# Kernel optimization log

Hardware: AMD Instinct MI355X
Metric: run time of the kernel (lower is better)

## Reference

```python
import jax, jax.numpy as jnp
import numpy as np

B, T, E, H, L = 8, 4096, 1024, 16, 64  # batch, seq, embed, heads, local window
HD = E // H


def setup_inputs() -> dict:
    key = jax.random.key(0)
    ks = jax.random.split(key, 5)
    s = 1.0 / np.sqrt(E).astype(np.float32)
    x = jax.random.normal(ks[0], (B, T, E), dtype=jnp.float32)
    W_qkv = jax.random.normal(ks[1], (3 * E, E), dtype=jnp.float32) * s
    b_qkv = jnp.zeros((3 * E,), dtype=jnp.float32)
    W_out = jax.random.normal(ks[2], (E, E), dtype=jnp.float32) * s
    b_out = jnp.zeros((E,), dtype=jnp.float32)
    return {"x": x, "W_qkv": W_qkv, "b_qkv": b_qkv, "W_out": W_out, "b_out": b_out}


def reference(x, W_qkv, b_qkv, W_out, b_out):
    b, t, e = x.shape
    scaling = HD ** (-0.5)
    # T is already a multiple of L, so need_pad = 0 (matches torch path)
    qkv = x @ W_qkv.T + b_qkv                      # (B,T,3E)
    q, k, v = jnp.split(qkv, 3, axis=-1)           # each (B,T,E)
    q = q * scaling

    def to_blocks(a):
        # (B,T,E) -> (B,H,T/L,L,HD); matches torch view/transpose sequence
        return a.reshape(b, t, H, HD).transpose(0, 2, 1, 3).reshape(b, H, t // L, L, HD)

    qb, kb, vb = to_blocks(q), to_blocks(k), to_blocks(v)
    attn = jax.nn.softmax(jnp.einsum('bhnld,bhnmd->bhnlm', qb, kb), axis=-1)
    out = jnp.einsum('bhnlm,bhnmd->bhnld', attn, vb)  # (B,H,N,L,HD)
    out = out.reshape(b, H, t, HD).transpose(0, 2, 1, 3).reshape(b, t, e)
    return out @ W_out.T + b_out
```

## Files before the change

kernel.cpp:

```cpp
#include <hip/hip_runtime.h>
#include <hip/hip_bf16.h>

typedef __hip_bfloat16 bf16;
typedef __attribute__((ext_vector_type(8))) short short8;
typedef __attribute__((ext_vector_type(4))) float f32x4;

__device__ __forceinline__ void gload_lds16(const void* g, void* l) {
    __builtin_amdgcn_global_load_lds(
        (const __attribute__((address_space(1))) void*)g,
        (__attribute__((address_space(3))) void*)l, 16, 0, 0);
}

__device__ __forceinline__ void store_out(bf16* p, float v)  { *p = __float2bfloat16(v); }
__device__ __forceinline__ void store_out(float* p, float v) { *p = v; }

__global__ __launch_bounds__(256)
void cvt_f32_bf16(const float* __restrict__ in, bf16* __restrict__ out, long n)
{
    const long i = ((long)blockIdx.x * 256 + threadIdx.x) * 8;
    if (i + 8 > n) return;
    float4 a = *(const float4*)(in + i);
    float4 b = *(const float4*)(in + i + 4);
    bf16 o[8];
    o[0] = __float2bfloat16(a.x); o[1] = __float2bfloat16(a.y);
    o[2] = __float2bfloat16(a.z); o[3] = __float2bfloat16(a.w);
    o[4] = __float2bfloat16(b.x); o[5] = __float2bfloat16(b.y);
    o[6] = __float2bfloat16(b.z); o[7] = __float2bfloat16(b.w);
    *(uint4*)(out + i) = *(const uint4*)o;
}

template <typename OutT>
__global__ __launch_bounds__(512, 2)
void gemm256(const bf16* __restrict__ A, const bf16* __restrict__ Bt,
             const float* __restrict__ bias, OutT* __restrict__ C,
             int N, int K, int gxt)
{
    __shared__ bf16 As[4][8192];
    __shared__ bf16 Bs[4][8192];

    const int nwg  = gridDim.x;
    const int orig = blockIdx.x;
    const int qq = nwg >> 3, rr = nwg & 7, xc = orig & 7;
    const int wg = (xc < rr ? xc * (qq + 1) : rr * (qq + 1) + (xc - rr) * qq)
                 + (orig >> 3);
    const long m0 = (long)(wg / gxt) * 256;
    const long n0 = (long)(wg % gxt) * 256;

    const int tid = threadIdx.x;
    const int wv  = tid >> 6;
    const int ln  = tid & 63;
    const int l15 = ln & 15;
    const int qd  = ln >> 4;
    const int wm  = wv >> 2, wn = wv & 3;

    const int sl = (qd ^ ((l15 >> 1) & 3)) << 3;

    const int r0  = tid >> 2;
    const int c0s = (((tid & 3) ^ ((tid >> 3) & 3))) << 3;
    const bf16* gA0 = A  + (m0 + r0) * K + c0s;
    const bf16* gA1 = A  + (m0 + 128 + r0) * K + c0s;
    const bf16* gB0 = Bt + (n0 + r0) * K + c0s;
    const bf16* gB1 = Bt + (n0 + 128 + r0) * K + c0s;
    const int lw = wv * 512;

    const int NT = K >> 5;

#define STAGE_A(bb, src) do { \
        gload_lds16(gA0 + (src) * 32, &As[bb][lw]); \
        gload_lds16(gA1 + (src) * 32, &As[bb][4096 + lw]); } while (0)
#define STAGE_B(bb, src) do { \
        gload_lds16(gB0 + (src) * 32, &Bs[bb][lw]); \
        gload_lds16(gB1 + (src) * 32, &Bs[bb][4096 + lw]); } while (0)

    {
        const int s1 = 1 < NT ? 1 : 0;
        const int s2 = 2 < NT ? 2 : 0;
        STAGE_A(0, 0);  STAGE_B(0, 0);
        STAGE_A(1, s1); STAGE_B(1, s1);
        STAGE_A(2, s2); STAGE_B(2, s2);
    }

    f32x4 acc[8][4] = {};

    for (int kt = 0; kt < NT; ++kt) {
        const int b   = kt & 3;
        const int ks  = kt + 3;
        const int bb  = ks & 3;
        const int src = ks < NT ? ks : 0;

        asm volatile("s_waitcnt vmcnt(8)" ::: "memory");
        __builtin_amdgcn_s_barrier();
        asm volatile("" ::: "memory");

        const bf16* Ab = As[b];
        const bf16* Bb = Bs[b];

        short8 af[4], bf[4];
#pragma unroll
        for (int mi = 0; mi < 4; ++mi)
            af[mi] = *(const short8*)&Ab[(wm * 128 + mi * 16 + l15) * 32 + sl];
#pragma unroll
        for (int ni = 0; ni < 4; ++ni)
            bf[ni] = *(const short8*)&Bb[(wn * 64 + ni * 16 + l15) * 32 + sl];
        STAGE_A(bb, src);
        __builtin_amdgcn_s_barrier();
        asm volatile("s_waitcnt lgkmcnt(0)" ::: "memory");
        __builtin_amdgcn_sched_barrier(0);
        __builtin_amdgcn_s_setprio(1);
#pragma unroll
        for (int mi = 0; mi < 4; ++mi)
#pragma unroll
            for (int ni = 0; ni < 4; ++ni)
                acc[mi][ni] = __builtin_amdgcn_mfma_f32_16x16x32_bf16(
                    af[mi], bf[ni], acc[mi][ni], 0, 0, 0);
        __builtin_amdgcn_s_setprio(0);

#pragma unroll
        for (int mi = 0; mi < 4; ++mi)
            af[mi] = *(const short8*)&Ab[(wm * 128 + (mi + 4) * 16 + l15) * 32 + sl];
        STAGE_B(bb, src);
        __builtin_amdgcn_s_barrier();
        asm volatile("s_waitcnt lgkmcnt(0)" ::: "memory");
        __builtin_amdgcn_sched_barrier(0);
        __builtin_amdgcn_s_setprio(1);
#pragma unroll
        for (int mi = 0; mi < 4; ++mi)
#pragma unroll
            for (int ni = 0; ni < 4; ++ni)
                acc[mi + 4][ni] = __builtin_amdgcn_mfma_f32_16x16x32_bf16(
                    af[mi], bf[ni], acc[mi + 4][ni], 0, 0, 0);
        __builtin_amdgcn_s_setprio(0);
    }
#undef STAGE_A
#undef STAGE_B

    const long ccol = n0 + wn * 64;
    float bsv[4];
#pragma unroll
    for (int ni = 0; ni < 4; ++ni)
        bsv[ni] = bias[ccol + ni * 16 + l15];
#pragma unroll
    for (int mi = 0; mi < 8; ++mi) {
#pragma unroll
        for (int r = 0; r < 4; ++r) {
            const long row = m0 + wm * 128 + mi * 16 + qd * 4 + r;
            OutT* cp = C + row * N + ccol + l15;
#pragma unroll
            for (int ni = 0; ni < 4; ++ni)
                store_out(cp + ni * 16, acc[mi][ni][r] + bsv[ni]);
        }
    }
}

#define LROW 72

__global__ __launch_bounds__(256)
void attn_local(const bf16* __restrict__ qkv, bf16* __restrict__ out)
{
    __shared__ bf16 Qs[64 * LROW];
    __shared__ bf16 Ks[64 * LROW];
    __shared__ bf16 Vt[64 * LROW];
    __shared__ bf16 Ps[64 * LROW];

    const int cb = blockIdx.x;
    const int h  = blockIdx.y;
    const int tid = threadIdx.x;

    const long qoff = (long)cb * 64 * 3072 + h * 64;

#pragma unroll
    for (int p = 0; p < 2; ++p) {
        const int e = (p * 256 + tid) * 8;
        const int tk = e >> 6, cl = e & 63;
        const long g = qoff + (long)tk * 3072 + cl;
        *(uint4*)&Qs[tk * LROW + cl] = *(const uint4*)&qkv[g];
        *(uint4*)&Ks[tk * LROW + cl] = *(const uint4*)&qkv[g + 1024];
        uint4 vv = *(const uint4*)&qkv[g + 2048];
        const bf16* vp = (const bf16*)&vv;
#pragma unroll
        for (int j = 0; j < 8; ++j)
            Vt[(cl + j) * LROW + tk] = vp[j];
    }
    __syncthreads();

    const int wv = tid >> 6, ln = tid & 63, l15 = ln & 15, qd = ln >> 4;

    f32x4 sacc[4] = {};
#pragma unroll
    for (int kk = 0; kk < 64; kk += 32) {
        short8 aq = *(const short8*)&Qs[(wv * 16 + l15) * LROW + kk + qd * 8];
#pragma unroll
        for (int ni = 0; ni < 4; ++ni) {
            short8 bk = *(const short8*)&Ks[(ni * 16 + l15) * LROW + kk + qd * 8];
            sacc[ni] = __builtin_amdgcn_mfma_f32_16x16x32_bf16(aq, bk, sacc[ni], 0, 0, 0);
        }
    }

    float linv[4];
#pragma unroll
    for (int r = 0; r < 4; ++r) {
        float m = -3.4e38f;
#pragma unroll
        for (int ni = 0; ni < 4; ++ni) m = fmaxf(m, sacc[ni][r]);
#pragma unroll
        for (int off = 1; off < 16; off <<= 1) m = fmaxf(m, __shfl_xor(m, off));
        float s = 0.f, pv[4];
#pragma unroll
        for (int ni = 0; ni < 4; ++ni) {
            pv[ni] = __expf(0.125f * (sacc[ni][r] - m));
            s += pv[ni];
        }
#pragma unroll
        for (int off = 1; off < 16; off <<= 1) s += __shfl_xor(s, off);
        linv[r] = 1.f / s;
        const int row = wv * 16 + qd * 4 + r;
#pragma unroll
        for (int ni = 0; ni < 4; ++ni)
            Ps[row * LROW + ni * 16 + l15] = __float2bfloat16(pv[ni]);
    }
    __syncthreads();

    f32x4 oacc[4] = {};
#pragma unroll
    for (int kk = 0; kk < 64; kk += 32) {
        short8 ap = *(const short8*)&Ps[(wv * 16 + l15) * LROW + kk + qd * 8];
#pragma unroll
        for (int ni = 0; ni < 4; ++ni) {
            short8 bv = *(const short8*)&Vt[(ni * 16 + l15) * LROW + kk + qd * 8];
            oacc[ni] = __builtin_amdgcn_mfma_f32_16x16x32_bf16(ap, bv, oacc[ni], 0, 0, 0);
        }
    }

    const long obase = (long)cb * 64 * 1024 + h * 64;
#pragma unroll
    for (int r = 0; r < 4; ++r) {
        const int row = wv * 16 + qd * 4 + r;
#pragma unroll
        for (int ni = 0; ni < 4; ++ni)
            out[obase + (long)row * 1024 + ni * 16 + l15] =
                __float2bfloat16(oacc[ni][r] * linv[r]);
    }
}

extern "C" void kernel_launch(void* const* d_in, const int* in_sizes, int n_in,
                              void* d_out, int out_size, void* d_ws, size_t ws_size,
                              hipStream_t stream) {
    const float* x     = (const float*)d_in[0];
    const float* W_qkv = (const float*)d_in[1];
    const float* b_qkv = (const float*)d_in[2];
    const float* W_out = (const float*)d_in[3];
    const float* b_out = (const float*)d_in[4];
    float* out = (float*)d_out;

    bf16* Wqkv_b = (bf16*)d_ws;
    bf16* Wout_b = Wqkv_b + (size_t)3072 * 1024;
    bf16* chunk0 = Wout_b + (size_t)1024 * 1024;
    const size_t fixed_bytes = ((size_t)3072 * 1024 + (size_t)1024 * 1024) * 2;

    static const int cands[8] = {32768, 16384, 8192, 4096, 2048, 1024, 512, 256};
    int CH = 256;
    for (int i = 0; i < 8; ++i)
        if (fixed_bytes + (size_t)cands[i] * 10240 <= ws_size) { CH = cands[i]; break; }

    bf16* xb    = chunk0;
    bf16* qkvb  = xb + (size_t)CH * 1024;
    bf16* attnb = qkvb + (size_t)CH * 3072;

    const dim3 blk(256);
    const dim3 gblk(512);

    cvt_f32_bf16<<<dim3((3072 * 1024) / 2048), blk, 0, stream>>>(W_qkv, Wqkv_b, 3072 * 1024);
    cvt_f32_bf16<<<dim3((1024 * 1024) / 2048), blk, 0, stream>>>(W_out, Wout_b, 1024 * 1024);

    const int mt = CH / 256;

    for (int c0 = 0; c0 < 32768; c0 += CH) {
        const long ne = (long)CH * 1024;
        cvt_f32_bf16<<<dim3((int)(ne / 2048)), blk, 0, stream>>>(x + (size_t)c0 * 1024, xb, ne);
        gemm256<bf16><<<dim3(mt * (3072 / 256)), gblk, 0, stream>>>(
            xb, Wqkv_b, b_qkv, qkvb, 3072, 1024, 3072 / 256);
        attn_local<<<dim3(CH / 64, 16), blk, 0, stream>>>(qkvb, attnb);
        gemm256<float><<<dim3(mt * (1024 / 256)), gblk, 0, stream>>>(
            attnb, Wout_b, b_out, out + (size_t)c0 * 1024, 1024, 1024, 1024 / 256);
    }
}
```

Measured before the change: 586.5 us.

## Software-pipeline LDS fragment loads across k-tiles in the bf16 GEMM loop

The GEMM main loop now loads the next k-tile's A and B fragments from LDS while the current MFMAs run. It ping-pongs two B register sets and unrolls the loop by two. The per-iteration synchronisation drops from three barriers to one, with a looser vmcnt wait. The goal is to hide LDS read latency and barrier stalls behind matrix-core work. In exchange it uses more registers and drops the guards for small K, so it assumes at least three k-tiles and an even tile count.

```diff
diff --git a/kernel.cpp b/kernel.cpp
--- a/kernel.cpp
+++ b/kernel.cpp
@@ -72,65 +72,77 @@
         gload_lds16(gB0 + (src) * 32, &Bs[bb][lw]); \
         gload_lds16(gB1 + (src) * 32, &Bs[bb][4096 + lw]); } while (0)
 
-    {
-        const int s1 = 1 < NT ? 1 : 0;
-        const int s2 = 2 < NT ? 2 : 0;
-        STAGE_A(0, 0);  STAGE_B(0, 0);
-        STAGE_A(1, s1); STAGE_B(1, s1);
-        STAGE_A(2, s2); STAGE_B(2, s2);
-    }
+    STAGE_A(0, 0);  STAGE_B(0, 0);
+    STAGE_A(1, 1);  STAGE_B(1, 1);
+    STAGE_A(2, 2);  STAGE_B(2, 2);
 
     f32x4 acc[8][4] = {};
-
-    for (int kt = 0; kt < NT; ++kt) {
-        const int b   = kt & 3;
-        const int ks  = kt + 3;
-        const int bb  = ks & 3;
-        const int src = ks < NT ? ks : 0;
-
-        asm volatile("s_waitcnt vmcnt(8)" ::: "memory");
-        __builtin_amdgcn_s_barrier();
-        asm volatile("" ::: "memory");
-
-        const bf16* Ab = As[b];
-        const bf16* Bb = Bs[b];
-
-        short8 af[4], bf[4];
-#pragma unroll
-        for (int mi = 0; mi < 4; ++mi)
-            af[mi] = *(const short8*)&Ab[(wm * 128 + mi * 16 + l15) * 32 + sl];
-#pragma unroll
-        for (int ni = 0; ni < 4; ++ni)
-            bf[ni] = *(const short8*)&Bb[(wn * 64 + ni * 16 + l15) * 32 + sl];
-        STAGE_A(bb, src);
-        __builtin_amdgcn_s_barrier();
-        asm volatile("s_waitcnt lgkmcnt(0)" ::: "memory");
-        __builtin_amdgcn_sched_barrier(0);
-        __builtin_amdgcn_s_setprio(1);
-#pragma unroll
-        for (int mi = 0; mi < 4; ++mi)
-#pragma unroll
-            for (int ni = 0; ni < 4; ++ni)
-                acc[mi][ni] = __builtin_amdgcn_mfma_f32_16x16x32_bf16(
-                    af[mi], bf[ni], acc[mi][ni], 0, 0, 0);
-        __builtin_amdgcn_s_setprio(0);
-
-#pragma unroll
-        for (int mi = 0; mi < 4; ++mi)
-            af[mi] = *(const short8*)&Ab[(wm * 128 + (mi + 4) * 16 + l15) * 32 + sl];
-        STAGE_B(bb, src);
-        __builtin_amdgcn_s_barrier();
-        asm volatile("s_waitcnt lgkmcnt(0)" ::: "memory");
-        __builtin_amdgcn_sched_barrier(0);
-        __builtin_amdgcn_s_setprio(1);
-#pragma unroll
-        for (int mi = 0; mi < 4; ++mi)
-#pragma unroll
-            for (int ni = 0; ni < 4; ++ni)
-                acc[mi + 4][ni] = __builtin_amdgcn_mfma_f32_16x16x32_bf16(
-                    af[mi], bf[ni], acc[mi + 4][ni], 0, 0, 0);
-        __builtin_amdgcn_s_setprio(0);
-    }
+    short8 a0[4], a1[4], bA[4], bB[4];
+
+    asm volatile("s_waitcnt vmcnt(8)" ::: "memory");
+    __builtin_amdgcn_s_barrier();
+#pragma unroll
+    for (int mi = 0; mi < 4; ++mi)
+        a0[mi] = *(const short8*)&As[0][(wm * 128 + mi * 16 + l15) * 32 + sl];
+#pragma unroll
+    for (int ni = 0; ni < 4; ++ni)
+        bA[ni] = *(const short8*)&Bs[0][(wn * 64 + ni * 16 + l15) * 32 + sl];
+    asm volatile("s_waitcnt lgkmcnt(0)" ::: "memory");
+    __builtin_amdgcn_sched_barrier(0);
+
+#define GBODY(KT, BC, BN)                                                     \
+    {                                                                         \
+        asm volatile("s_waitcnt vmcnt(4)" ::: "memory");                      \
+        __builtin_amdgcn_s_barrier();                                         \
+        const int b_  = (KT) & 3;                                             \
+        const int ks_ = (KT) + 3;                                             \
+        const int bb_ = ks_ & 3;                                              \
+        const int sr_ = ks_ < NT ? ks_ : 0;                                   \
+        const bf16* Ab_ = As[b_];                                             \
+        const bf16* An_ = As[((KT) + 1) & 3];                                 \
+        const bf16* Bn_ = Bs[((KT) + 1) & 3];                                 \
+        _Pragma("unroll")                                                     \
+        for (int mi = 0; mi < 4; ++mi)                                        \
+            a1[mi] = *(const short8*)&Ab_[(wm * 128 + (mi + 4) * 16 + l15) * 32 + sl]; \
+        gload_lds16(gA0 + sr_ * 32, &As[bb_][lw]);                            \
+        gload_lds16(gA1 + sr_ * 32, &As[bb_][4096 + lw]);                     \
+        __builtin_amdgcn_sched_barrier(0);                                    \
+        __builtin_amdgcn_s_setprio(1);                                        \
+        _Pragma("unroll")                                                     \
+        for (int mi = 0; mi < 4; ++mi)                                        \
+            _Pragma("unroll")                                                 \
+            for (int ni = 0; ni < 4; ++ni)                                    \
+                acc[mi][ni] = __builtin_amdgcn_mfma_f32_16x16x32_bf16(        \
+                    a0[mi], BC[ni], acc[mi][ni], 0, 0, 0);                    \
+        __builtin_amdgcn_s_setprio(0);                                        \
+        asm volatile("s_waitcnt lgkmcnt(0)" ::: "memory");                    \
+        __builtin_amdgcn_sched_barrier(0);                                    \
+        _Pragma("unroll")                                                     \
+        for (int mi = 0; mi < 4; ++mi)                                        \
+            a0[mi] = *(const short8*)&An_[(wm * 128 + mi * 16 + l15) * 32 + sl]; \
+        _Pragma("unroll")                                                     \
+        for (int ni = 0; ni < 4; ++ni)                                        \
+            BN[ni] = *(const short8*)&Bn_[(wn * 64 + ni * 16 + l15) * 32 + sl]; \
+        gload_lds16(gB0 + sr_ * 32, &Bs[bb_][lw]);                            \
+        gload_lds16(gB1 + sr_ * 32, &Bs[bb_][4096 + lw]);                     \
+        __builtin_amdgcn_sched_barrier(0);                                    \
+        __builtin_amdgcn_s_setprio(1);                                        \
+        _Pragma("unroll")                                                     \
+        for (int mi = 0; mi < 4; ++mi)                                        \
+            _Pragma("unroll")                                                 \
+            for (int ni = 0; ni < 4; ++ni)                                    \
+                acc[mi + 4][ni] = __builtin_amdgcn_mfma_f32_16x16x32_bf16(    \
+                    a1[mi], BC[ni], acc[mi + 4][ni], 0, 0, 0);                \
+        __builtin_amdgcn_s_setprio(0);                                        \
+        asm volatile("s_waitcnt lgkmcnt(0)" ::: "memory");                    \
+        __builtin_amdgcn_sched_barrier(0);                                    \
+    }
+
+    for (int kt = 0; kt < NT; kt += 2) {
+        GBODY(kt,     bA, bB);
+        GBODY(kt + 1, bB, bA);
+    }
+#undef GBODY
 #undef STAGE_A
 #undef STAGE_B
 
```

Result: slower. 603.2 us (+2.8%).
